# Kernel optimization log

Hardware: AMD Instinct MI355X
Metric: run time of the kernel (lower is better)

Reference implementation:

```python
import jax, jax.numpy as jnp
import numpy as np

DIM = 256
HEADS = 8
WS = 7  # window_size
EPS = 1e-5


def dwconv1d(x, w, b):
    # x: (B, Cg, L); w: (Cg, 1, k); depthwise (groups=Cg), 'same' padding for odd k
    k = w.shape[-1]
    p = k // 2
    y = jax.lax.conv_general_dilated(
        x, w, window_strides=(1,), padding=[(p, p)],
        dimension_numbers=('NCH', 'OIH', 'NCH'),
        feature_group_count=x.shape[1])
    return y + b[None, :, None]


def group_norm(x, scale, bias, groups):
    # x: (B, C, *spatial); normalize over (C//groups, *spatial) per group
    B, C = x.shape[0], x.shape[1]
    xg = x.reshape(B, groups, -1)
    mean = xg.mean(-1, keepdims=True)
    var = xg.var(-1, keepdims=True)
    xn = ((xg - mean) * jax.lax.rsqrt(var + EPS)).reshape(x.shape)
    bshape = (1, C) + (1,) * (x.ndim - 2)
    return xn * scale.reshape(bshape) + bias.reshape(bshape)


def setup_inputs() -> dict:
    key = jax.random.key(0)
    ks = jax.random.split(key, 16)
    gc = DIM // 4
    d = {"x": jax.random.normal(ks[0], (32, DIM, 56, 56), dtype=jnp.float32)}
    for i, k in enumerate([3, 5, 7, 9]):
        d[f"w_dwc{k}"] = jax.random.normal(ks[1 + i], (gc, 1, k), dtype=jnp.float32) * (1.0 / np.sqrt(k))
        d[f"b_dwc{k}"] = jax.random.normal(ks[5 + i], (gc,), dtype=jnp.float32) * 0.02
    d["norm_h_scale"] = jnp.ones((DIM,), jnp.float32)
    d["norm_h_bias"] = jnp.zeros((DIM,), jnp.float32)
    d["norm_w_scale"] = jnp.ones((DIM,), jnp.float32)
    d["norm_w_bias"] = jnp.zeros((DIM,), jnp.float32)
    d["norm_scale"] = jnp.ones((DIM,), jnp.float32)
    d["norm_bias"] = jnp.zeros((DIM,), jnp.float32)
    d["q_w"] = jax.random.normal(ks[9], (DIM,), dtype=jnp.float32)
    d["k_w"] = jax.random.normal(ks[10], (DIM,), dtype=jnp.float32)
    d["v_w"] = jax.random.normal(ks[11], (DIM,), dtype=jnp.float32)
    return d


def reference(x, w_dwc3, b_dwc3, w_dwc5, b_dwc5, w_dwc7, b_dwc7, w_dwc9, b_dwc9,
              norm_h_scale, norm_h_bias, norm_w_scale, norm_w_bias,
              norm_scale, norm_bias, q_w, k_w, v_w):
    b, c, h, w = x.shape
    head_dim = c // HEADS

    def sa_branch(xm, scale, bias):
        # xm: (B, C, L) -> sigmoid(GroupNorm4(concat of 4 depthwise convs))
        p0, p1, p2, p3 = jnp.split(xm, 4, axis=1)
        y = jnp.concatenate([
            dwconv1d(p0, w_dwc3, b_dwc3),
            dwconv1d(p1, w_dwc5, b_dwc5),
            dwconv1d(p2, w_dwc7, b_dwc7),
            dwconv1d(p3, w_dwc9, b_dwc9)], axis=1)
        return jax.nn.sigmoid(group_norm(y, scale, bias, 4))

    x_h_attn = sa_branch(x.mean(axis=3), norm_h_scale, norm_h_bias)[:, :, :, None]  # (B,C,H,1)
    x_w_attn = sa_branch(x.mean(axis=2), norm_w_scale, norm_w_bias)[:, :, None, :]  # (B,C,1,W)
    xg = x * x_h_attn * x_w_attn

    # AvgPool2d(WS, stride=WS)
    hs, ws_ = h // WS, w // WS
    y = xg.reshape(b, c, hs, WS, ws_, WS).mean(axis=(3, 5))  # (B,C,hs,ws)
    y = group_norm(y, norm_scale, norm_bias, 1)

    n = hs * ws_
    q = (y * q_w[None, :, None, None]).reshape(b, HEADS, head_dim, n)
    k = (y * k_w[None, :, None, None]).reshape(b, HEADS, head_dim, n)
    v = (y * v_w[None, :, None, None]).reshape(b, HEADS, head_dim, n)

    attn = jnp.einsum('bhdn,bhen->bhde', q, k) * (head_dim ** -0.5)
    attn = jax.nn.softmax(attn, axis=-1)
    out = jnp.einsum('bhde,bhen->bhdn', attn, v)  # (B,H,hd,n)

    ca = jax.nn.sigmoid(out.reshape(b, c, n).mean(axis=-1))[:, :, None, None]  # (B,C,1,1)
    return ca * xg
```

## Files before the change

kernel.cpp:

```cpp
#include <hip/hip_runtime.h>
#include <hip/hip_cooperative_groups.h>
#include <cstdint>
#include <cstddef>

namespace cg = cooperative_groups;

#define NB 32
#define NC 256
#define HW 56
#define PLANE (HW*HW)
#define NPLANE (NB*NC)
#define NHEADS 8
#define HDIM 32
#define NPOOL 64
#define EPSV 1e-5f
#define NBLK 1024
#define PPB (NPLANE/NBLK)
#define NUM_CU 256

struct Ph13 { float buf[PLANE]; float ha[56]; float wa[56]; };
struct Ph2  { float rows[64*57]; float red[8]; };
struct Ph4  { float yn[32][65]; float G[32][33]; float ybar[32]; float red[8]; float stats[2]; };
struct Ph5  { float hv[8][56]; float wv[8][56]; };
union SmemU { Ph13 a; Ph2 b; Ph4 c; Ph5 d; };

template<int K>
__device__ __forceinline__ void ph2_work(const float* __restrict__ src,
                                         const float* __restrict__ wk,
                                         const float* __restrict__ bk,
                                         const float* __restrict__ scale,
                                         const float* __restrict__ bias,
                                         float* __restrict__ dst,
                                         int cbase, Ph2* S2, int t) {
    const float4* sp = (const float4*)src;
#pragma unroll
    for (int k2 = 0; k2 < 4; ++k2) {
        int f = t + 256 * k2;
        if (f < 896) {
            float4 v = sp[f];
            int c = f / 14, r = f - c * 14;
            float* d = &S2->rows[c * 57 + r * 4];
            d[0] = v.x; d[1] = v.y; d[2] = v.z; d[3] = v.w;
        }
    }
    __syncthreads();
    int cc = t >> 2, q = t & 3;
    float w[K];
#pragma unroll
    for (int j = 0; j < K; ++j) w[j] = wk[cc * K + j];
    float bb = bk[cc];
    const float* row = &S2->rows[cc * 57];
    float y[14];
    float s1 = 0.f, s2 = 0.f;
#pragma unroll
    for (int il = 0; il < 14; ++il) {
        int pos = q * 14 + il;
        float a = bb;
#pragma unroll
        for (int j = 0; j < K; ++j) {
            int p2 = pos + j - K / 2;
            if (p2 >= 0 && p2 < 56) a += w[j] * row[p2];
        }
        y[il] = a; s1 += a; s2 += a * a;
    }
#pragma unroll
    for (int off = 32; off >= 1; off >>= 1) {
        s1 += __shfl_xor(s1, off);
        s2 += __shfl_xor(s2, off);
    }
    int wv = t >> 6;
    if ((t & 63) == 0) { S2->red[wv] = s1; S2->red[4 + wv] = s2; }
    __syncthreads();
    float t1 = S2->red[0] + S2->red[1] + S2->red[2] + S2->red[3];
    float t2 = S2->red[4] + S2->red[5] + S2->red[6] + S2->red[7];
    float mean = t1 * (1.f / 3584.f);
    float var = t2 * (1.f / 3584.f) - mean * mean;
    float rstd = rsqrtf(var + EPSV);
    int c = cbase + cc;
    float scv = scale[c];
    float a_lin = scv * rstd, b_lin = bias[c] - mean * rstd * scv;
#pragma unroll
    for (int il = 0; il < 14; ++il) {
        float v = y[il] * a_lin + b_lin;
        S2->rows[cc * 57 + q * 14 + il] = 1.f / (1.f + expf(-v));
    }
    __syncthreads();
    float4* dp = (float4*)dst;
#pragma unroll
    for (int k2 = 0; k2 < 4; ++k2) {
        int f = t + 256 * k2;
        if (f < 896) {
            int c2 = f / 14, r = f - c2 * 14;
            const float* s = &S2->rows[c2 * 57 + r * 4];
            dp[f] = make_float4(s[0], s[1], s[2], s[3]);
        }
    }
}

__global__ __launch_bounds__(256, 4) void k_mega(
    const float* __restrict__ x,
    const float* __restrict__ w3, const float* __restrict__ b3,
    const float* __restrict__ w5, const float* __restrict__ b5,
    const float* __restrict__ w7, const float* __restrict__ b7,
    const float* __restrict__ w9, const float* __restrict__ b9,
    const float* __restrict__ hsc, const float* __restrict__ hbi,
    const float* __restrict__ wsc, const float* __restrict__ wbi,
    const float* __restrict__ nsc, const float* __restrict__ nbi,
    const float* __restrict__ qw, const float* __restrict__ kw,
    const float* __restrict__ vw,
    float* __restrict__ hm, float* __restrict__ wm,
    float* __restrict__ hattn, float* __restrict__ wattn,
    float* __restrict__ ypool, float* __restrict__ ca,
    float* __restrict__ out)
{
    cg::grid_group grid = cg::this_grid();
    __shared__ SmemU S;
    const int t = threadIdx.x;
    const int bid = blockIdx.x;

    for (int p = 0; p < PPB; ++p) {
        int plane = bid * PPB + p;
        {
            const float4* xp = (const float4*)(x + (size_t)plane * PLANE);
            float4* smp = (float4*)S.a.buf;
            for (int f = t; f < PLANE / 4; f += 256) smp[f] = xp[f];
        }
        __syncthreads();
        const float* sm = S.a.buf;
        if (t < 224) {
            int a = t >> 2, q = t & 3;
            float s = 0.f;
#pragma unroll
            for (int i = 0; i < 14; ++i) s += sm[a * 56 + q * 14 + i];
            s += __shfl_xor(s, 1); s += __shfl_xor(s, 2);
            if (q == 0) hm[(size_t)plane * 56 + a] = s * (1.f / 56.f);
            float s2 = 0.f;
#pragma unroll
            for (int i = 0; i < 14; ++i) s2 += sm[(q * 14 + i) * 56 + a];
            s2 += __shfl_xor(s2, 1); s2 += __shfl_xor(s2, 2);
            if (q == 0) wm[(size_t)plane * 56 + a] = s2 * (1.f / 56.f);
        }
        __syncthreads();
    }
    grid.sync();

    if (bid < 256) {
        int mode = bid & 1, b = (bid >> 1) & 31, g = bid >> 6;
        const float* src = (mode ? wm : hm) + ((size_t)b * NC + g * 64) * 56;
        float* dst = (mode ? wattn : hattn) + ((size_t)b * NC + g * 64) * 56;
        const float* scale = mode ? wsc : hsc;
        const float* bias = mode ? wbi : hbi;
        switch (g) {
            case 0: ph2_work<3>(src, w3, b3, scale, bias, dst, 0,   &S.b, t); break;
            case 1: ph2_work<5>(src, w5, b5, scale, bias, dst, 64,  &S.b, t); break;
            case 2: ph2_work<7>(src, w7, b7, scale, bias, dst, 128, &S.b, t); break;
            default: ph2_work<9>(src, w9, b9, scale, bias, dst, 192, &S.b, t); break;
        }
    }
    grid.sync();

    for (int p = 0; p < PPB; ++p) {
        int plane = bid * PPB + p;
        {
            const float4* xp = (const float4*)(x + (size_t)plane * PLANE);
            float4* smp = (float4*)S.a.buf;
            for (int f = t; f < PLANE / 4; f += 256) smp[f] = xp[f];
            if (t < 56) S.a.ha[t] = hattn[(size_t)plane * 56 + t];
            else if (t >= 64 && t < 120) S.a.wa[t - 64] = wattn[(size_t)plane * 56 + (t - 64)];
        }
        __syncthreads();
        {
            const float* sm = S.a.buf;
            const float* ha = S.a.ha;
            const float* wa = S.a.wa;
            int cell = t >> 2, sub = t & 3;
            int i = cell >> 3, j = cell & 7;
            float s = 0.f;
#pragma unroll
            for (int k2 = 0; k2 < 2; ++k2) {
                int dh = sub + 4 * k2;
                if (dh < 7) {
                    float r = 0.f;
#pragma unroll
                    for (int dw = 0; dw < 7; ++dw)
                        r += sm[(7 * i + dh) * 56 + 7 * j + dw] * wa[7 * j + dw];
                    s += ha[7 * i + dh] * r;
                }
            }
            s += __shfl_xor(s, 1); s += __shfl_xor(s, 2);
            if (sub == 0) ypool[(size_t)plane * NPOOL + cell] = s * (1.f / 49.f);
        }
        __syncthreads();
    }
    grid.sync();

    if (bid < 256) {
        int b = bid >> 3, h = bid & 7;
        const float4* bp4 = (const float4*)(ypool + (size_t)b * NC * NPOOL);
        float s1 = 0.f, s2 = 0.f;
#pragma unroll
        for (int k2 = 0; k2 < 16; ++k2) {
            float4 v = bp4[t + 256 * k2];
            s1 += v.x + v.y + v.z + v.w;
            s2 += v.x * v.x + v.y * v.y + v.z * v.z + v.w * v.w;
        }
#pragma unroll
        for (int off = 32; off >= 1; off >>= 1) {
            s1 += __shfl_xor(s1, off);
            s2 += __shfl_xor(s2, off);
        }
        if ((t & 63) == 0) { S.c.red[t >> 6] = s1; S.c.red[4 + (t >> 6)] = s2; }
        __syncthreads();
        if (t == 0) {
            float t1 = S.c.red[0] + S.c.red[1] + S.c.red[2] + S.c.red[3];
            float t2 = S.c.red[4] + S.c.red[5] + S.c.red[6] + S.c.red[7];
            float mean = t1 * (1.f / (NC * NPOOL));
            float var = t2 * (1.f / (NC * NPOOL)) - mean * mean;
            S.c.stats[0] = mean; S.c.stats[1] = rsqrtf(var + EPSV);
        }
        __syncthreads();
        float mean = S.c.stats[0], rstd = S.c.stats[1];
        const float* base = ypool + ((size_t)b * NC + h * HDIM) * NPOOL;
#pragma unroll
        for (int m = 0; m < 8; ++m) {
            int idx = t + 256 * m;
            int d = idx >> 6, p = idx & 63;
            int ch = h * HDIM + d;
            S.c.yn[d][p] = (base[idx] - mean) * rstd * nsc[ch] + nbi[ch];
        }
        __syncthreads();
        if (t < 32) {
            float s = 0.f;
#pragma unroll
            for (int p = 0; p < 64; ++p) s += S.c.yn[t][p];
            S.c.ybar[t] = s * (1.f / 64.f);
        }
        __syncthreads();
#pragma unroll
        for (int m = 0; m < 4; ++m) {
            int idx = t + 256 * m;
            int d = idx >> 5, e = idx & 31;
            float s = 0.f;
#pragma unroll
            for (int p = 0; p < 64; ++p) s += S.c.yn[d][p] * S.c.yn[e][p];
            S.c.G[d][e] = s;
        }
        __syncthreads();
        if (t < 32) {
            int d = t, cd = h * HDIM + d;
            float qs = qw[cd] * 0.17677669529663687f;
            float a[32];
            float mx = -1e30f;
#pragma unroll
            for (int e = 0; e < 32; ++e) {
                a[e] = S.c.G[d][e] * qs * kw[h * HDIM + e];
                mx = fmaxf(mx, a[e]);
            }
            float sum = 0.f;
#pragma unroll
            for (int e = 0; e < 32; ++e) {
                a[e] = expf(a[e] - mx);
                sum += a[e];
            }
            float o = 0.f;
#pragma unroll
            for (int e = 0; e < 32; ++e) o += a[e] * vw[h * HDIM + e] * S.c.ybar[e];
            o /= sum;
            ca[b * NC + cd] = 1.f / (1.f + expf(-o));
        }
    }
    grid.sync();

    {
        for (int i = t; i < 448; i += 256) {
            int p = i / 56, a = i - p * 56;
            int pl = bid * PPB + p;
            S.d.hv[p][a] = hattn[(size_t)pl * 56 + a] * ca[pl];
            S.d.wv[p][a] = wattn[(size_t)pl * 56 + a];
        }
        __syncthreads();
        for (int p = 0; p < PPB; ++p) {
            int plane = bid * PPB + p;
            const float* hv = S.d.hv[p];
            const float* wv = S.d.wv[p];
            const float4* xp = (const float4*)(x + (size_t)plane * PLANE);
            float4* op = (float4*)(out + (size_t)plane * PLANE);
            for (int f = t; f < PLANE / 4; f += 256) {
                int r = f / 14, s0 = (f - r * 14) * 4;
                float4 v = xp[f];
                float hf = hv[r];
                v.x *= hf * wv[s0];
                v.y *= hf * wv[s0 + 1];
                v.z *= hf * wv[s0 + 2];
                v.w *= hf * wv[s0 + 3];
                op[f] = v;
            }
        }
    }
}

__global__ __launch_bounds__(256) void k_means(const float* __restrict__ x,
                                               float* __restrict__ hm,
                                               float* __restrict__ wm) {
    int plane = blockIdx.x;
    __shared__ float sm[PLANE];
    const float4* xp = (const float4*)(x + (size_t)plane * PLANE);
    float4* smp = (float4*)sm;
    int t = threadIdx.x;
    for (int f = t; f < PLANE / 4; f += 256) smp[f] = xp[f];
    __syncthreads();
    if (t < 224) {
        int a = t >> 2, q = t & 3;
        float s = 0.f;
#pragma unroll
        for (int i = 0; i < 14; ++i) s += sm[a * 56 + q * 14 + i];
        s += __shfl_xor(s, 1); s += __shfl_xor(s, 2);
        if (q == 0) hm[(size_t)plane * 56 + a] = s * (1.f / 56.f);
        float s2 = 0.f;
#pragma unroll
        for (int i = 0; i < 14; ++i) s2 += sm[(q * 14 + i) * 56 + a];
        s2 += __shfl_xor(s2, 1); s2 += __shfl_xor(s2, 2);
        if (q == 0) wm[(size_t)plane * 56 + a] = s2 * (1.f / 56.f);
    }
}

__global__ __launch_bounds__(256) void k_branch(
    const float* __restrict__ hm, const float* __restrict__ wm,
    const float* __restrict__ w3, const float* __restrict__ b3,
    const float* __restrict__ w5, const float* __restrict__ b5,
    const float* __restrict__ w7, const float* __restrict__ b7,
    const float* __restrict__ w9, const float* __restrict__ b9,
    const float* __restrict__ hsc, const float* __restrict__ hbi,
    const float* __restrict__ wsc, const float* __restrict__ wbi,
    float* __restrict__ hattn, float* __restrict__ wattn) {
    int mode = blockIdx.x & 1;
    int b = blockIdx.x >> 1;
    const float* src = (mode == 0 ? hm : wm) + (size_t)b * NC * 56;
    const float* scale = (mode == 0 ? hsc : wsc);
    const float* bias = (mode == 0 ? hbi : wbi);
    float* dst = (mode == 0 ? hattn : wattn) + (size_t)b * NC * 56;

    __shared__ float sm[NC * 57];
    int t = threadIdx.x;
    const float4* sp = (const float4*)src;
#pragma unroll
    for (int k = 0; k < 14; ++k) {
        int f = t + 256 * k;
        float4 v = sp[f];
        int c = f / 14, r = f - c * 14;
        float* d = &sm[c * 57 + r * 4];
        d[0] = v.x; d[1] = v.y; d[2] = v.z; d[3] = v.w;
    }
    __syncthreads();

    int c = t;
    int g = c >> 6, cc = c & 63;
    float wc[9];
#pragma unroll
    for (int i = 0; i < 9; ++i) wc[i] = 0.f;
    float bb = 0.f;
    if (g == 0) {
#pragma unroll
        for (int q = 0; q < 3; ++q) wc[3 + q] = w3[cc * 3 + q];
        bb = b3[cc];
    } else if (g == 1) {
#pragma unroll
        for (int q = 0; q < 5; ++q) wc[2 + q] = w5[cc * 5 + q];
        bb = b5[cc];
    } else if (g == 2) {
#pragma unroll
        for (int q = 0; q < 7; ++q) wc[1 + q] = w7[cc * 7 + q];
        bb = b7[cc];
    } else {
#pragma unroll
        for (int q = 0; q < 9; ++q) wc[q] = w9[cc * 9 + q];
        bb = b9[cc];
    }

    float xv[56];
#pragma unroll
    for (int i = 0; i < 56; ++i) xv[i] = sm[c * 57 + i];

    float s1 = 0.f, s2 = 0.f;
#pragma unroll
    for (int i = 0; i < 56; ++i) {
        float a = bb;
#pragma unroll
        for (int d = 0; d < 9; ++d) {
            int j = i + d - 4;
            if (j >= 0 && j < 56) a += wc[d] * xv[j];
        }
        s1 += a;
        s2 += a * a;
    }
#pragma unroll
    for (int off = 32; off >= 1; off >>= 1) {
        s1 += __shfl_xor(s1, off);
        s2 += __shfl_xor(s2, off);
    }
    float mean = s1 * (1.f / 3584.f);
    float var = s2 * (1.f / 3584.f) - mean * mean;
    float rstd = rsqrtf(var + EPSV);
    float scv = scale[c];
    float a_lin = scv * rstd;
    float b_lin = bias[c] - mean * rstd * scv;
#pragma unroll
    for (int i = 0; i < 56; ++i) {
        float a = bb;
#pragma unroll
        for (int d = 0; d < 9; ++d) {
            int j = i + d - 4;
            if (j >= 0 && j < 56) a += wc[d] * xv[j];
        }
        float v = a * a_lin + b_lin;
        sm[c * 57 + i] = 1.f / (1.f + expf(-v));
    }
    __syncthreads();
    float4* dp = (float4*)dst;
#pragma unroll
    for (int k = 0; k < 14; ++k) {
        int f = t + 256 * k;
        int c2 = f / 14, r = f - c2 * 14;
        const float* s = &sm[c2 * 57 + r * 4];
        dp[f] = make_float4(s[0], s[1], s[2], s[3]);
    }
}

__global__ __launch_bounds__(256) void k_pool(const float* __restrict__ x,
                                              const float* __restrict__ hattn,
                                              const float* __restrict__ wattn,
                                              float* __restrict__ ypool) {
    int plane = blockIdx.x;
    __shared__ float sm[PLANE];
    __shared__ float ha[56], wa[56];
    const float4* xp = (const float4*)(x + (size_t)plane * PLANE);
    float4* smp = (float4*)sm;
    int t = threadIdx.x;
    for (int f = t; f < PLANE / 4; f += 256) smp[f] = xp[f];
    if (t < 56) ha[t] = hattn[(size_t)plane * 56 + t];
    else if (t >= 64 && t < 120) wa[t - 64] = wattn[(size_t)plane * 56 + (t - 64)];
    __syncthreads();
    if (t < 64) {
        int i = t >> 3, j = t & 7;
        float s = 0.f;
#pragma unroll
        for (int dh = 0; dh < 7; ++dh) {
            float hv = ha[7 * i + dh];
            float r = 0.f;
#pragma unroll
            for (int dw = 0; dw < 7; ++dw)
                r += sm[(7 * i + dh) * 56 + 7 * j + dw] * wa[7 * j + dw];
            s += hv * r;
        }
        ypool[(size_t)plane * NPOOL + t] = s * (1.f / 49.f);
    }
}

__global__ __launch_bounds__(64) void k_attn(const float* __restrict__ ypool,
                                             const float* __restrict__ nsc,
                                             const float* __restrict__ nbi,
                                             const float* __restrict__ qw,
                                             const float* __restrict__ kw,
                                             const float* __restrict__ vw,
                                             float* __restrict__ ca) {
    int bh = blockIdx.x;
    int b = bh >> 3, h = bh & 7;
    int l = threadIdx.x;
    const float4* bp = (const float4*)(ypool + (size_t)b * NC * NPOOL);
    float s1 = 0.f, s2 = 0.f;
#pragma unroll
    for (int k = 0; k < 64; ++k) {
        float4 v = bp[l + 64 * k];
        s1 += v.x + v.y + v.z + v.w;
        s2 += v.x * v.x + v.y * v.y + v.z * v.z + v.w * v.w;
    }
#pragma unroll
    for (int off = 32; off >= 1; off >>= 1) {
        s1 += __shfl_xor(s1, off);
        s2 += __shfl_xor(s2, off);
    }
    float mean = s1 * (1.f / (NC * NPOOL));
    float var = s2 * (1.f / (NC * NPOOL)) - mean * mean;
    float rstd = rsqrtf(var + EPSV);

    __shared__ float yn[32][65];
    __shared__ float ybar[32];
    __shared__ float G[32][33];
    const float* base = ypool + ((size_t)b * NC + h * HDIM) * NPOOL;
#pragma unroll
    for (int m = 0; m < 32; ++m) {
        int idx = l + 64 * m;
        int d = idx >> 6, p = idx & 63;
        int ch = h * HDIM + d;
        float v = base[idx];
        yn[d][p] = (v - mean) * rstd * nsc[ch] + nbi[ch];
    }
    __syncthreads();
    if (l < 32) {
        float s = 0.f;
#pragma unroll
        for (int p = 0; p < 64; ++p) s += yn[l][p];
        ybar[l] = s * (1.f / 64.f);
    }
    __syncthreads();
#pragma unroll
    for (int m = 0; m < 16; ++m) {
        int idx = l + 64 * m;
        int d = idx >> 5, e = idx & 31;
        float s = 0.f;
#pragma unroll
        for (int p = 0; p < 64; ++p) s += yn[d][p] * yn[e][p];
        G[d][e] = s;
    }
    __syncthreads();
    if (l < 32) {
        int d = l, cd = h * HDIM + d;
        float qs = qw[cd] * 0.17677669529663687f;
        float a[32];
        float mx = -1e30f;
#pragma unroll
        for (int e = 0; e < 32; ++e) {
            a[e] = G[d][e] * qs * kw[h * HDIM + e];
            mx = fmaxf(mx, a[e]);
        }
        float sum = 0.f;
#pragma unroll
        for (int e = 0; e < 32; ++e) {
            a[e] = expf(a[e] - mx);
            sum += a[e];
        }
        float o = 0.f;
#pragma unroll
        for (int e = 0; e < 32; ++e) o += a[e] * vw[h * HDIM + e] * ybar[e];
        o /= sum;
        ca[b * NC + cd] = 1.f / (1.f + expf(-o));
    }
}

__global__ __launch_bounds__(256) void k_final(const float* __restrict__ x,
                                               const float* __restrict__ hattn,
                                               const float* __restrict__ wattn,
                                               const float* __restrict__ ca,
                                               float* __restrict__ out) {
    int plane = blockIdx.x;
    __shared__ float hv[56], wv[56];
    int t = threadIdx.x;
    float cav = ca[plane];
    if (t < 56) hv[t] = hattn[(size_t)plane * 56 + t] * cav;
    else if (t >= 64 && t < 120) wv[t - 64] = wattn[(size_t)plane * 56 + (t - 64)];
    __syncthreads();
    const float4* xp = (const float4*)(x + (size_t)plane * PLANE);
    float4* op = (float4*)(out + (size_t)plane * PLANE);
    for (int f = t; f < PLANE / 4; f += 256) {
        int r = f / 14;
        int s0 = (f - r * 14) * 4;
        float4 v = xp[f];
        float hf = hv[r];
        v.x *= hf * wv[s0];
        v.y *= hf * wv[s0 + 1];
        v.z *= hf * wv[s0 + 2];
        v.w *= hf * wv[s0 + 3];
        op[f] = v;
    }
}

extern "C" void kernel_launch(void* const* d_in, const int* in_sizes, int n_in,
                              void* d_out, int out_size, void* d_ws, size_t ws_size,
                              hipStream_t stream) {
    const float* x   = (const float*)d_in[0];
    const float* w3  = (const float*)d_in[1];
    const float* b3  = (const float*)d_in[2];
    const float* w5  = (const float*)d_in[3];
    const float* b5  = (const float*)d_in[4];
    const float* w7  = (const float*)d_in[5];
    const float* b7  = (const float*)d_in[6];
    const float* w9  = (const float*)d_in[7];
    const float* b9  = (const float*)d_in[8];
    const float* hsc = (const float*)d_in[9];
    const float* hbi = (const float*)d_in[10];
    const float* wsc = (const float*)d_in[11];
    const float* wbi = (const float*)d_in[12];
    const float* nsc = (const float*)d_in[13];
    const float* nbi = (const float*)d_in[14];
    const float* qw  = (const float*)d_in[15];
    const float* kw  = (const float*)d_in[16];
    const float* vw  = (const float*)d_in[17];
    float* out = (float*)d_out;

    float* ws    = (float*)d_ws;
    float* hm    = ws;
    float* wm    = hm + (size_t)NPLANE * 56;
    float* hattn = wm + (size_t)NPLANE * 56;
    float* wattn = hattn + (size_t)NPLANE * 56;
    float* ypool = wattn + (size_t)NPLANE * 56;
    float* ca    = ypool + (size_t)NPLANE * NPOOL;

    bool coop_done = false;
    int maxb = 0;
    hipError_t qe = hipOccupancyMaxActiveBlocksPerMultiprocessor(
        &maxb, (const void*)k_mega, 256, 0);
    if (qe == hipSuccess && maxb * NUM_CU >= NBLK) {
        void* args[] = {
            (void*)&x,
            (void*)&w3, (void*)&b3, (void*)&w5, (void*)&b5,
            (void*)&w7, (void*)&b7, (void*)&w9, (void*)&b9,
            (void*)&hsc, (void*)&hbi, (void*)&wsc, (void*)&wbi,
            (void*)&nsc, (void*)&nbi,
            (void*)&qw, (void*)&kw, (void*)&vw,
            (void*)&hm, (void*)&wm, (void*)&hattn, (void*)&wattn,
            (void*)&ypool, (void*)&ca, (void*)&out
        };
        hipError_t le = hipLaunchCooperativeKernel((const void*)k_mega, dim3(NBLK),
                                                   dim3(256), args, 0, stream);
        coop_done = (le == hipSuccess);
    }
    if (!coop_done) {
        (void)hipGetLastError();
        k_means<<<NPLANE, 256, 0, stream>>>(x, hm, wm);
        k_branch<<<2 * NB, 256, 0, stream>>>(hm, wm, w3, b3, w5, b5, w7, b7, w9, b9,
                                             hsc, hbi, wsc, wbi, hattn, wattn);
        k_pool<<<NPLANE, 256, 0, stream>>>(x, hattn, wattn, ypool);
        k_attn<<<NB * NHEADS, 64, 0, stream>>>(ypool, nsc, nbi, qw, kw, vw, ca);
        k_final<<<NPLANE, 256, 0, stream>>>(x, hattn, wattn, ca, out);
    }
}
```

Baseline: 285.7 us.

## Replace cooperative megakernel with separate launches using finer-grained per-phase parallelism

Removes the cooperative grid-synchronized megakernel and always runs the five-kernel pipeline. The branch, pool and attention kernels are rewritten to use the megakernel's finer work split: 256 branch blocks, 4 threads per pooled cell, and 256-thread attention blocks. This aims to eliminate grid.sync costs and the sequential per-block plane loop, letting more blocks stream x concurrently. In exchange it adds several kernel launch boundaries.

```diff
diff --git a/kernel.cpp b/kernel.cpp
--- a/kernel.cpp
+++ b/kernel.cpp
@@ -1,9 +1,6 @@
 #include <hip/hip_runtime.h>
-#include <hip/hip_cooperative_groups.h>
 #include <cstdint>
 #include <cstddef>
-
-namespace cg = cooperative_groups;
 
 #define NB 32
 #define NC 256
@@ -14,15 +11,8 @@
 #define HDIM 32
 #define NPOOL 64
 #define EPSV 1e-5f
-#define NBLK 1024
-#define PPB (NPLANE/NBLK)
-#define NUM_CU 256
-
-struct Ph13 { float buf[PLANE]; float ha[56]; float wa[56]; };
-struct Ph2  { float rows[64*57]; float red[8]; };
-struct Ph4  { float yn[32][65]; float G[32][33]; float ybar[32]; float red[8]; float stats[2]; };
-struct Ph5  { float hv[8][56]; float wv[8][56]; };
-union SmemU { Ph13 a; Ph2 b; Ph4 c; Ph5 d; };
+
+struct Ph2 { float rows[64*57]; float red[8]; };
 
 template<int K>
 __device__ __forceinline__ void ph2_work(const float* __restrict__ src,
@@ -97,208 +87,6 @@
     }
 }
 
-__global__ __launch_bounds__(256, 4) void k_mega(
-    const float* __restrict__ x,
-    const float* __restrict__ w3, const float* __restrict__ b3,
-    const float* __restrict__ w5, const float* __restrict__ b5,
-    const float* __restrict__ w7, const float* __restrict__ b7,
-    const float* __restrict__ w9, const float* __restrict__ b9,
-    const float* __restrict__ hsc, const float* __restrict__ hbi,
-    const float* __restrict__ wsc, const float* __restrict__ wbi,
-    const float* __restrict__ nsc, const float* __restrict__ nbi,
-    const float* __restrict__ qw, const float* __restrict__ kw,
-    const float* __restrict__ vw,
-    float* __restrict__ hm, float* __restrict__ wm,
-    float* __restrict__ hattn, float* __restrict__ wattn,
-    float* __restrict__ ypool, float* __restrict__ ca,
-    float* __restrict__ out)
-{
-    cg::grid_group grid = cg::this_grid();
-    __shared__ SmemU S;
-    const int t = threadIdx.x;
-    const int bid = blockIdx.x;
-
-    for (int p = 0; p < PPB; ++p) {
-        int plane = bid * PPB + p;
-        {
-            const float4* xp = (const float4*)(x + (size_t)plane * PLANE);
-            float4* smp = (float4*)S.a.buf;
-            for (int f = t; f < PLANE / 4; f += 256) smp[f] = xp[f];
-        }
-        __syncthreads();
-        const float* sm = S.a.buf;
-        if (t < 224) {
-            int a = t >> 2, q = t & 3;
-            float s = 0.f;
-#pragma unroll
-            for (int i = 0; i < 14; ++i) s += sm[a * 56 + q * 14 + i];
-            s += __shfl_xor(s, 1); s += __shfl_xor(s, 2);
-            if (q == 0) hm[(size_t)plane * 56 + a] = s * (1.f / 56.f);
-            float s2 = 0.f;
-#pragma unroll
-            for (int i = 0; i < 14; ++i) s2 += sm[(q * 14 + i) * 56 + a];
-            s2 += __shfl_xor(s2, 1); s2 += __shfl_xor(s2, 2);
-            if (q == 0) wm[(size_t)plane * 56 + a] = s2 * (1.f / 56.f);
-        }
-        __syncthreads();
-    }
-    grid.sync();
-
-    if (bid < 256) {
-        int mode = bid & 1, b = (bid >> 1) & 31, g = bid >> 6;
-        const float* src = (mode ? wm : hm) + ((size_t)b * NC + g * 64) * 56;
-        float* dst = (mode ? wattn : hattn) + ((size_t)b * NC + g * 64) * 56;
-        const float* scale = mode ? wsc : hsc;
-        const float* bias = mode ? wbi : hbi;
-        switch (g) {
-            case 0: ph2_work<3>(src, w3, b3, scale, bias, dst, 0,   &S.b, t); break;
-            case 1: ph2_work<5>(src, w5, b5, scale, bias, dst, 64,  &S.b, t); break;
-            case 2: ph2_work<7>(src, w7, b7, scale, bias, dst, 128, &S.b, t); break;
-            default: ph2_work<9>(src, w9, b9, scale, bias, dst, 192, &S.b, t); break;
-        }
-    }
-    grid.sync();
-
-    for (int p = 0; p < PPB; ++p) {
-        int plane = bid * PPB + p;
-        {
-            const float4* xp = (const float4*)(x + (size_t)plane * PLANE);
-            float4* smp = (float4*)S.a.buf;
-            for (int f = t; f < PLANE / 4; f += 256) smp[f] = xp[f];
-            if (t < 56) S.a.ha[t] = hattn[(size_t)plane * 56 + t];
-            else if (t >= 64 && t < 120) S.a.wa[t - 64] = wattn[(size_t)plane * 56 + (t - 64)];
-        }
-        __syncthreads();
-        {
-            const float* sm = S.a.buf;
-            const float* ha = S.a.ha;
-            const float* wa = S.a.wa;
-            int cell = t >> 2, sub = t & 3;
-            int i = cell >> 3, j = cell & 7;
-            float s = 0.f;
-#pragma unroll
-            for (int k2 = 0; k2 < 2; ++k2) {
-                int dh = sub + 4 * k2;
-                if (dh < 7) {
-                    float r = 0.f;
-#pragma unroll
-                    for (int dw = 0; dw < 7; ++dw)
-                        r += sm[(7 * i + dh) * 56 + 7 * j + dw] * wa[7 * j + dw];
-                    s += ha[7 * i + dh] * r;
-                }
-            }
-            s += __shfl_xor(s, 1); s += __shfl_xor(s, 2);
-            if (sub == 0) ypool[(size_t)plane * NPOOL + cell] = s * (1.f / 49.f);
-        }
-        __syncthreads();
-    }
-    grid.sync();
-
-    if (bid < 256) {
-        int b = bid >> 3, h = bid & 7;
-        const float4* bp4 = (const float4*)(ypool + (size_t)b * NC * NPOOL);
-        float s1 = 0.f, s2 = 0.f;
-#pragma unroll
-        for (int k2 = 0; k2 < 16; ++k2) {
-            float4 v = bp4[t + 256 * k2];
-            s1 += v.x + v.y + v.z + v.w;
-            s2 += v.x * v.x + v.y * v.y + v.z * v.z + v.w * v.w;
-        }
-#pragma unroll
-        for (int off = 32; off >= 1; off >>= 1) {
-            s1 += __shfl_xor(s1, off);
-            s2 += __shfl_xor(s2, off);
-        }
-        if ((t & 63) == 0) { S.c.red[t >> 6] = s1; S.c.red[4 + (t >> 6)] = s2; }
-        __syncthreads();
-        if (t == 0) {
-            float t1 = S.c.red[0] + S.c.red[1] + S.c.red[2] + S.c.red[3];
-            float t2 = S.c.red[4] + S.c.red[5] + S.c.red[6] + S.c.red[7];
-            float mean = t1 * (1.f / (NC * NPOOL));
-            float var = t2 * (1.f / (NC * NPOOL)) - mean * mean;
-            S.c.stats[0] = mean; S.c.stats[1] = rsqrtf(var + EPSV);
-        }
-        __syncthreads();
-        float mean = S.c.stats[0], rstd = S.c.stats[1];
-        const float* base = ypool + ((size_t)b * NC + h * HDIM) * NPOOL;
-#pragma unroll
-        for (int m = 0; m < 8; ++m) {
-            int idx = t + 256 * m;
-            int d = idx >> 6, p = idx & 63;
-            int ch = h * HDIM + d;
-            S.c.yn[d][p] = (base[idx] - mean) * rstd * nsc[ch] + nbi[ch];
-        }
-        __syncthreads();
-        if (t < 32) {
-            float s = 0.f;
-#pragma unroll
-            for (int p = 0; p < 64; ++p) s += S.c.yn[t][p];
-            S.c.ybar[t] = s * (1.f / 64.f);
-        }
-        __syncthreads();
-#pragma unroll
-        for (int m = 0; m < 4; ++m) {
-            int idx = t + 256 * m;
-            int d = idx >> 5, e = idx & 31;
-            float s = 0.f;
-#pragma unroll
-            for (int p = 0; p < 64; ++p) s += S.c.yn[d][p] * S.c.yn[e][p];
-            S.c.G[d][e] = s;
-        }
-        __syncthreads();
-        if (t < 32) {
-            int d = t, cd = h * HDIM + d;
-            float qs = qw[cd] * 0.17677669529663687f;
-            float a[32];
-            float mx = -1e30f;
-#pragma unroll
-            for (int e = 0; e < 32; ++e) {
-                a[e] = S.c.G[d][e] * qs * kw[h * HDIM + e];
-                mx = fmaxf(mx, a[e]);
-            }
-            float sum = 0.f;
-#pragma unroll
-            for (int e = 0; e < 32; ++e) {
-                a[e] = expf(a[e] - mx);
-                sum += a[e];
-            }
-            float o = 0.f;
-#pragma unroll
-            for (int e = 0; e < 32; ++e) o += a[e] * vw[h * HDIM + e] * S.c.ybar[e];
-            o /= sum;
-            ca[b * NC + cd] = 1.f / (1.f + expf(-o));
-        }
-    }
-    grid.sync();
-
-    {
-        for (int i = t; i < 448; i += 256) {
-            int p = i / 56, a = i - p * 56;
-            int pl = bid * PPB + p;
-            S.d.hv[p][a] = hattn[(size_t)pl * 56 + a] * ca[pl];
-            S.d.wv[p][a] = wattn[(size_t)pl * 56 + a];
-        }
-        __syncthreads();
-        for (int p = 0; p < PPB; ++p) {
-            int plane = bid * PPB + p;
-            const float* hv = S.d.hv[p];
-            const float* wv = S.d.wv[p];
-            const float4* xp = (const float4*)(x + (size_t)plane * PLANE);
-            float4* op = (float4*)(out + (size_t)plane * PLANE);
-            for (int f = t; f < PLANE / 4; f += 256) {
-                int r = f / 14, s0 = (f - r * 14) * 4;
-                float4 v = xp[f];
-                float hf = hv[r];
-                v.x *= hf * wv[s0];
-                v.y *= hf * wv[s0 + 1];
-                v.z *= hf * wv[s0 + 2];
-                v.w *= hf * wv[s0 + 3];
-                op[f] = v;
-            }
-        }
-    }
-}
-
 __global__ __launch_bounds__(256) void k_means(const float* __restrict__ x,
                                                float* __restrict__ hm,
                                                float* __restrict__ wm) {
@@ -333,96 +121,18 @@
     const float* __restrict__ hsc, const float* __restrict__ hbi,
     const float* __restrict__ wsc, const float* __restrict__ wbi,
     float* __restrict__ hattn, float* __restrict__ wattn) {
-    int mode = blockIdx.x & 1;
-    int b = blockIdx.x >> 1;
-    const float* src = (mode == 0 ? hm : wm) + (size_t)b * NC * 56;
-    const float* scale = (mode == 0 ? hsc : wsc);
-    const float* bias = (mode == 0 ? hbi : wbi);
-    float* dst = (mode == 0 ? hattn : wattn) + (size_t)b * NC * 56;
-
-    __shared__ float sm[NC * 57];
-    int t = threadIdx.x;
-    const float4* sp = (const float4*)src;
-#pragma unroll
-    for (int k = 0; k < 14; ++k) {
-        int f = t + 256 * k;
-        float4 v = sp[f];
-        int c = f / 14, r = f - c * 14;
-        float* d = &sm[c * 57 + r * 4];
-        d[0] = v.x; d[1] = v.y; d[2] = v.z; d[3] = v.w;
-    }
-    __syncthreads();
-
-    int c = t;
-    int g = c >> 6, cc = c & 63;
-    float wc[9];
-#pragma unroll
-    for (int i = 0; i < 9; ++i) wc[i] = 0.f;
-    float bb = 0.f;
-    if (g == 0) {
-#pragma unroll
-        for (int q = 0; q < 3; ++q) wc[3 + q] = w3[cc * 3 + q];
-        bb = b3[cc];
-    } else if (g == 1) {
-#pragma unroll
-        for (int q = 0; q < 5; ++q) wc[2 + q] = w5[cc * 5 + q];
-        bb = b5[cc];
-    } else if (g == 2) {
-#pragma unroll
-        for (int q = 0; q < 7; ++q) wc[1 + q] = w7[cc * 7 + q];
-        bb = b7[cc];
-    } else {
-#pragma unroll
-        for (int q = 0; q < 9; ++q) wc[q] = w9[cc * 9 + q];
-        bb = b9[cc];
-    }
-
-    float xv[56];
-#pragma unroll
-    for (int i = 0; i < 56; ++i) xv[i] = sm[c * 57 + i];
-
-    float s1 = 0.f, s2 = 0.f;
-#pragma unroll
-    for (int i = 0; i < 56; ++i) {
-        float a = bb;
-#pragma unroll
-        for (int d = 0; d < 9; ++d) {
-            int j = i + d - 4;
-            if (j >= 0 && j < 56) a += wc[d] * xv[j];
-        }
-        s1 += a;
-        s2 += a * a;
-    }
-#pragma unroll
-    for (int off = 32; off >= 1; off >>= 1) {
-        s1 += __shfl_xor(s1, off);
-        s2 += __shfl_xor(s2, off);
-    }
-    float mean = s1 * (1.f / 3584.f);
-    float var = s2 * (1.f / 3584.f) - mean * mean;
-    float rstd = rsqrtf(var + EPSV);
-    float scv = scale[c];
-    float a_lin = scv * rstd;
-    float b_lin = bias[c] - mean * rstd * scv;
-#pragma unroll
-    for (int i = 0; i < 56; ++i) {
-        float a = bb;
-#pragma unroll
-        for (int d = 0; d < 9; ++d) {
-            int j = i + d - 4;
-            if (j >= 0 && j < 56) a += wc[d] * xv[j];
-        }
-        float v = a * a_lin + b_lin;
-        sm[c * 57 + i] = 1.f / (1.f + expf(-v));
-    }
-    __syncthreads();
-    float4* dp = (float4*)dst;
-#pragma unroll
-    for (int k = 0; k < 14; ++k) {
-        int f = t + 256 * k;
-        int c2 = f / 14, r = f - c2 * 14;
-        const float* s = &sm[c2 * 57 + r * 4];
-        dp[f] = make_float4(s[0], s[1], s[2], s[3]);
+    __shared__ Ph2 S2;
+    int t = threadIdx.x, bid = blockIdx.x;
+    int mode = bid & 1, b = (bid >> 1) & 31, g = bid >> 6;
+    const float* src = (mode ? wm : hm) + ((size_t)b * NC + g * 64) * 56;
+    float* dst = (mode ? wattn : hattn) + ((size_t)b * NC + g * 64) * 56;
+    const float* scale = mode ? wsc : hsc;
+    const float* bias = mode ? wbi : hbi;
+    switch (g) {
+        case 0: ph2_work<3>(src, w3, b3, scale, bias, dst, 0,   &S2, t); break;
+        case 1: ph2_work<5>(src, w5, b5, scale, bias, dst, 64,  &S2, t); break;
+        case 2: ph2_work<7>(src, w7, b7, scale, bias, dst, 128, &S2, t); break;
+        default: ph2_work<9>(src, w9, b9, scale, bias, dst, 192, &S2, t); break;
     }
 }
 
@@ -440,37 +150,44 @@
     if (t < 56) ha[t] = hattn[(size_t)plane * 56 + t];
     else if (t >= 64 && t < 120) wa[t - 64] = wattn[(size_t)plane * 56 + (t - 64)];
     __syncthreads();
-    if (t < 64) {
-        int i = t >> 3, j = t & 7;
-        float s = 0.f;
-#pragma unroll
-        for (int dh = 0; dh < 7; ++dh) {
-            float hv = ha[7 * i + dh];
+    int cell = t >> 2, sub = t & 3;
+    int i = cell >> 3, j = cell & 7;
+    float s = 0.f;
+#pragma unroll
+    for (int k2 = 0; k2 < 2; ++k2) {
+        int dh = sub + 4 * k2;
+        if (dh < 7) {
             float r = 0.f;
 #pragma unroll
             for (int dw = 0; dw < 7; ++dw)
                 r += sm[(7 * i + dh) * 56 + 7 * j + dw] * wa[7 * j + dw];
-            s += hv * r;
-        }
-        ypool[(size_t)plane * NPOOL + t] = s * (1.f / 49.f);
-    }
-}
-
-__global__ __launch_bounds__(64) void k_attn(const float* __restrict__ ypool,
-                                             const float* __restrict__ nsc,
-                                             const float* __restrict__ nbi,
-                                             const float* __restrict__ qw,
-                                             const float* __restrict__ kw,
-                                             const float* __restrict__ vw,
-                                             float* __restrict__ ca) {
-    int bh = blockIdx.x;
-    int b = bh >> 3, h = bh & 7;
-    int l = threadIdx.x;
-    const float4* bp = (const float4*)(ypool + (size_t)b * NC * NPOOL);
+            s += ha[7 * i + dh] * r;
+        }
+    }
+    s += __shfl_xor(s, 1); s += __shfl_xor(s, 2);
+    if (sub == 0) ypool[(size_t)plane * NPOOL + cell] = s * (1.f / 49.f);
+}
+
+__global__ __launch_bounds__(256) void k_attn(const float* __restrict__ ypool,
+                                              const float* __restrict__ nsc,
+                                              const float* __restrict__ nbi,
+                                              const float* __restrict__ qw,
+                                              const float* __restrict__ kw,
+                                              const float* __restrict__ vw,
+                                              float* __restrict__ ca) {
+    int b = blockIdx.x >> 3, h = blockIdx.x & 7;
+    int t = threadIdx.x;
+    __shared__ float yn[32][65];
+    __shared__ float G[32][33];
+    __shared__ float ybar[32];
+    __shared__ float red[8];
+    __shared__ float stats[2];
+
+    const float4* bp4 = (const float4*)(ypool + (size_t)b * NC * NPOOL);
     float s1 = 0.f, s2 = 0.f;
 #pragma unroll
-    for (int k = 0; k < 64; ++k) {
-        float4 v = bp[l + 64 * k];
+    for (int k2 = 0; k2 < 16; ++k2) {
+        float4 v = bp4[t + 256 * k2];
         s1 += v.x + v.y + v.z + v.w;
         s2 += v.x * v.x + v.y * v.y + v.z * v.z + v.w * v.w;
     }
@@ -479,33 +196,36 @@
         s1 += __shfl_xor(s1, off);
         s2 += __shfl_xor(s2, off);
     }
-    float mean = s1 * (1.f / (NC * NPOOL));
-    float var = s2 * (1.f / (NC * NPOOL)) - mean * mean;
-    float rstd = rsqrtf(var + EPSV);
-
-    __shared__ float yn[32][65];
-    __shared__ float ybar[32];
-    __shared__ float G[32][33];
+    if ((t & 63) == 0) { red[t >> 6] = s1; red[4 + (t >> 6)] = s2; }
+    __syncthreads();
+    if (t == 0) {
+        float t1 = red[0] + red[1] + red[2] + red[3];
+        float t2 = red[4] + red[5] + red[6] + red[7];
+        float mean = t1 * (1.f / (NC * NPOOL));
+        float var = t2 * (1.f / (NC * NPOOL)) - mean * mean;
+        stats[0] = mean; stats[1] = rsqrtf(var + EPSV);
+    }
+    __syncthreads();
+    float mean = stats[0], rstd = stats[1];
     const float* base = ypool + ((size_t)b * NC + h * HDIM) * NPOOL;
 #pragma unroll
-    for (int m = 0; m < 32; ++m) {
-        int idx = l + 64 * m;
+    for (int m = 0; m < 8; ++m) {
+        int idx = t + 256 * m;
         int d = idx >> 6, p = idx & 63;
         int ch = h * HDIM + d;
-        float v = base[idx];
-        yn[d][p] = (v - mean) * rstd * nsc[ch] + nbi[ch];
-    }
-    __syncthreads();
-    if (l < 32) {
+        yn[d][p] = (base[idx] - mean) * rstd * nsc[ch] + nbi[ch];
+    }
+    __syncthreads();
+    if (t < 32) {
         float s = 0.f;
 #pragma unroll
-        for (int p = 0; p < 64; ++p) s += yn[l][p];
-        ybar[l] = s * (1.f / 64.f);
-    }
-    __syncthreads();
-#pragma unroll
-    for (int m = 0; m < 16; ++m) {
-        int idx = l + 64 * m;
+        for (int p = 0; p < 64; ++p) s += yn[t][p];
+        ybar[t] = s * (1.f / 64.f);
+    }
+    __syncthreads();
+#pragma unroll
+    for (int m = 0; m < 4; ++m) {
+        int idx = t + 256 * m;
         int d = idx >> 5, e = idx & 31;
         float s = 0.f;
 #pragma unroll
@@ -513,8 +233,8 @@
         G[d][e] = s;
     }
     __syncthreads();
-    if (l < 32) {
-        int d = l, cd = h * HDIM + d;
+    if (t < 32) {
+        int d = t, cd = h * HDIM + d;
         float qs = qw[cd] * 0.17677669529663687f;
         float a[32];
         float mx = -1e30f;
@@ -595,32 +315,10 @@
     float* ypool = wattn + (size_t)NPLANE * 56;
     float* ca    = ypool + (size_t)NPLANE * NPOOL;
 
-    bool coop_done = false;
-    int maxb = 0;
-    hipError_t qe = hipOccupancyMaxActiveBlocksPerMultiprocessor(
-        &maxb, (const void*)k_mega, 256, 0);
-    if (qe == hipSuccess && maxb * NUM_CU >= NBLK) {
-        void* args[] = {
-            (void*)&x,
-            (void*)&w3, (void*)&b3, (void*)&w5, (void*)&b5,
-            (void*)&w7, (void*)&b7, (void*)&w9, (void*)&b9,
-            (void*)&hsc, (void*)&hbi, (void*)&wsc, (void*)&wbi,
-            (void*)&nsc, (void*)&nbi,
-            (void*)&qw, (void*)&kw, (void*)&vw,
-            (void*)&hm, (void*)&wm, (void*)&hattn, (void*)&wattn,
-            (void*)&ypool, (void*)&ca, (void*)&out
-        };
-        hipError_t le = hipLaunchCooperativeKernel((const void*)k_mega, dim3(NBLK),
-                                                   dim3(256), args, 0, stream);
-        coop_done = (le == hipSuccess);
-    }
-    if (!coop_done) {
-        (void)hipGetLastError();
-        k_means<<<NPLANE, 256, 0, stream>>>(x, hm, wm);
-        k_branch<<<2 * NB, 256, 0, stream>>>(hm, wm, w3, b3, w5, b5, w7, b7, w9, b9,
-                                             hsc, hbi, wsc, wbi, hattn, wattn);
-        k_pool<<<NPLANE, 256, 0, stream>>>(x, hattn, wattn, ypool);
-        k_attn<<<NB * NHEADS, 64, 0, stream>>>(ypool, nsc, nbi, qw, kw, vw, ca);
-        k_final<<<NPLANE, 256, 0, stream>>>(x, hattn, wattn, ca, out);
-    }
-}
+    k_means<<<NPLANE, 256, 0, stream>>>(x, hm, wm);
+    k_branch<<<256, 256, 0, stream>>>(hm, wm, w3, b3, w5, b5, w7, b7, w9, b9,
+                                      hsc, hbi, wsc, wbi, hattn, wattn);
+    k_pool<<<NPLANE, 256, 0, stream>>>(x, hattn, wattn, ypool);
+    k_attn<<<NB * NHEADS, 256, 0, stream>>>(ypool, nsc, nbi, qw, kw, vw, ca);
+    k_final<<<NPLANE, 256, 0, stream>>>(x, hattn, wattn, ca, out);
+}
```

Result: faster. 260.3 us (-8.9%).
